# Kernel optimization log

Hardware: AMD Instinct MI355X
Metric: run time of the kernel (lower is better)

The kernel has to match this reference:

```python
import math
import jax, jax.numpy as jnp
import numpy as np

CT = {"SDD": 1000.0, "SCD": 500.0, "det_interval": 1.0, "num_det": 736}


def ramp_filter_np(ct, scale):
    # Standard equiangular fan-beam ramp filter (utility.ramp_filter):
    #   h[0] = 1/(8*db^2); h[n odd] = -1/(2*(pi*sin(n*db))^2); h[n even!=0] = 0
    db = ct["det_interval"] / ct["SDD"] * scale  # angular detector pitch at this scale
    n_det = int(ct["num_det"] // scale)
    n = np.arange(-(n_det - 1), n_det)  # length K = 2*n_det - 1
    h = np.zeros(n.shape, dtype=np.float32)
    h[n == 0] = 1.0 / (8.0 * db ** 2)
    odd = (n % 2) != 0
    h[odd] = -0.5 / (np.pi * np.sin(n[odd] * db)) ** 2
    return h


def setup_inputs() -> dict:
    key = jax.random.key(0)
    scale = 1
    batch, ch, view, det = 16, 1, 1152, CT["num_det"] // scale
    sinogram = jax.random.normal(key, (batch, ch, view, det), dtype=jnp.float32)
    delta_b = CT["det_interval"] / CT["SDD"]
    # recon_filter = ramp_filter * scale * delta_b, shaped [1,1,1,K] (OIHW)
    filt = ramp_filter_np(CT, scale) * scale * delta_b
    recon_filter = jnp.asarray(filt, dtype=jnp.float32)[None, None, None, :]
    return {"sinogram": sinogram, "recon_filter": recon_filter, "scale": scale}


def reference(sinogram, recon_filter, scale):
    det = sinogram.shape[-1]
    # cosine fan-beam pre-weighting
    s_range = (CT["det_interval"]
               * jnp.linspace((1.0 - det) / 2.0, (det - 1.0) / 2.0, det, dtype=jnp.float32)
               * scale) / CT["SDD"]
    cos_weight = (CT["SCD"] / 10000.0) * jnp.cos(s_range)  # [det]
    x = sinogram * cos_weight[None, None, None, :]
    # 1D ramp-filter convolution along detector axis (F.conv2d with 1xK kernel)
    K = recon_filter.shape[-1]
    pad = K // 2
    out = jax.lax.conv_general_dilated(
        x, recon_filter,
        window_strides=(1, 1),
        padding=[(0, 0), (pad, pad)],
        dimension_numbers=("NCHW", "OIHW", "NCHW"),
    )
    return out
```

## Files before the change

### kernel.cpp

```cpp
#include <hip/hip_runtime.h>

typedef unsigned short ushort_t;
typedef ushort_t u16x8 __attribute__((ext_vector_type(8)));
typedef __bf16 bf16x8 __attribute__((ext_vector_type(8)));
typedef float f32x4 __attribute__((ext_vector_type(4)));

#define DET 736
#define NPAD 768
#define NT 23

__device__ __forceinline__ ushort_t f2bf(float f) {
    unsigned u = __builtin_bit_cast(unsigned, f);
    u += 0x7FFFu + ((u >> 16) & 1u);
    return (ushort_t)(u >> 16);
}

__device__ __forceinline__ void gload16(const void* g, void* l) {
    __builtin_amdgcn_global_load_lds(
        (const __attribute__((address_space(1))) unsigned int*)g,
        (__attribute__((address_space(3))) unsigned int*)l,
        16, 0, 0);
}

__global__ void prep_bt(const float* __restrict__ filt, ushort_t* __restrict__ Bt) {
    int idx = blockIdx.x * blockDim.x + threadIdx.x;
    if (idx >= NPAD * DET) return;
    int n = idx / DET;
    int k = idx - n * DET;
    float w = 0.05f * cosf(((float)k - 367.5f) * 0.001f);
    float v = (n < DET) ? filt[k - n + (DET - 1)] * w : 0.0f;
    Bt[idx] = f2bf(v);
}

__global__ __launch_bounds__(256, 4) void gemm_fused(
    const float* __restrict__ A,
    const ushort_t* __restrict__ Bt,
    float* __restrict__ C, int M)
{
    __shared__ ushort_t As[128 * 32];
    __shared__ ushort_t Bs[128 * 32];

    const int tid  = threadIdx.x;
    const int lane = tid & 63;
    const int warp = tid >> 6;
    const int wm   = warp & 1;
    const int wn   = warp >> 1;
    const int quad = lane >> 4;
    const int l16  = lane & 15;

    const size_t row_a0 = (size_t)blockIdx.x * 128;
    const int    row_b0 = blockIdx.y * 128;

    f32x4 acc[4][4];
#pragma unroll
    for (int i = 0; i < 4; ++i)
#pragma unroll
        for (int jx = 0; jx < 4; ++jx)
            acc[i][jx] = (f32x4){0.f, 0.f, 0.f, 0.f};

    const int c0 = tid, c1 = tid + 256;
    const int r0 = c0 >> 2, q0 = c0 & 3;
    const int r1 = c1 >> 2, q1 = c1 & 3;

    const float*    gA0 = A + (row_a0 + r0) * DET + q0 * 8;
    const float*    gA1 = A + (row_a0 + r1) * DET + q1 * 8;
    const ushort_t* gB0 = Bt + (size_t)(row_b0 + r0) * DET + q0 * 8;
    const ushort_t* gB1 = Bt + (size_t)(row_b0 + r1) * DET + q1 * 8;

    f32x4 a0lo = *(const f32x4*)(gA0);
    f32x4 a0hi = *(const f32x4*)(gA0 + 4);
    f32x4 a1lo = *(const f32x4*)(gA1);
    f32x4 a1hi = *(const f32x4*)(gA1 + 4);

    for (int t = 0; t < NT; ++t) {
        __syncthreads();

        u16x8 oa0, oa1;
#pragma unroll
        for (int e = 0; e < 4; ++e) {
            oa0[e]     = f2bf(a0lo[e]);
            oa0[e + 4] = f2bf(a0hi[e]);
            oa1[e]     = f2bf(a1lo[e]);
            oa1[e + 4] = f2bf(a1hi[e]);
        }
        *(u16x8*)(As + c0 * 8) = oa0;
        *(u16x8*)(As + c1 * 8) = oa1;

        const int k0 = t * 32;
        gload16(gB0 + k0, Bs + c0 * 8);
        gload16(gB1 + k0, Bs + c1 * 8);

        __syncthreads();

        if (t + 1 < NT) {
            const int kn = (t + 1) * 32;
            a0lo = *(const f32x4*)(gA0 + kn);
            a0hi = *(const f32x4*)(gA0 + kn + 4);
            a1lo = *(const f32x4*)(gA1 + kn);
            a1hi = *(const f32x4*)(gA1 + kn + 4);
        }

        u16x8 af[4], bfr[4];
#pragma unroll
        for (int mi = 0; mi < 4; ++mi)
            af[mi] = *(const u16x8*)(As + (wm * 64 + mi * 16 + l16) * 32 + quad * 8);
#pragma unroll
        for (int ni = 0; ni < 4; ++ni)
            bfr[ni] = *(const u16x8*)(Bs + (wn * 64 + ni * 16 + l16) * 32 + quad * 8);
#pragma unroll
        for (int mi = 0; mi < 4; ++mi)
#pragma unroll
            for (int ni = 0; ni < 4; ++ni)
                acc[mi][ni] = __builtin_amdgcn_mfma_f32_16x16x32_bf16(
                    __builtin_bit_cast(bf16x8, af[mi]),
                    __builtin_bit_cast(bf16x8, bfr[ni]),
                    acc[mi][ni], 0, 0, 0);
    }

#pragma unroll
    for (int mi = 0; mi < 4; ++mi) {
#pragma unroll
        for (int ni = 0; ni < 4; ++ni) {
            int colg = row_b0 + wn * 64 + ni * 16 + l16;
            if (colg < DET) {
#pragma unroll
                for (int r = 0; r < 4; ++r) {
                    size_t rowg = row_a0 + wm * 64 + mi * 16 + quad * 4 + r;
                    C[rowg * DET + colg] = acc[mi][ni][r];
                }
            }
        }
    }
}

extern "C" void kernel_launch(void* const* d_in, const int* in_sizes, int n_in,
                              void* d_out, int out_size, void* d_ws, size_t ws_size,
                              hipStream_t stream) {
    const float* sino = (const float*)d_in[0];
    const float* filt = (const float*)d_in[1];
    int total = in_sizes[0];
    int M = total / DET;

    ushort_t* Btb = (ushort_t*)d_ws;
    float* out = (float*)d_out;

    prep_bt<<<(NPAD * DET + 255) / 256, 256, 0, stream>>>(filt, Btb);

    dim3 grid(M / 128, NPAD / 128);
    gemm_fused<<<grid, 256, 0, stream>>>(sino, Btb, out, M);
}
```

Before: 132.2 us.

## Double-buffer fp32 A tile in LDS with swizzle, load B fragments directly to registers

The GEMM now stages the fp32 sinogram tile straight into a double-buffered, XOR-swizzled LDS buffer with async global-to-LDS loads. It converts to bf16 at fragment read time and no longer converts in registers before the LDS store. The B (filter matrix) fragments are loaded from global memory directly into registers with a one-step prefetch, skipping LDS. Each K step now needs one barrier instead of two, so loads overlap compute. In exchange, LDS use doubles, register pressure rises, occupancy is lowered to 3 blocks, and each B fragment is read redundantly by the waves that share it.

```diff
diff --git a/kernel.cpp b/kernel.cpp
--- a/kernel.cpp
+++ b/kernel.cpp
@@ -32,13 +32,12 @@
     Bt[idx] = f2bf(v);
 }
 
-__global__ __launch_bounds__(256, 4) void gemm_fused(
+__global__ __launch_bounds__(256, 3) void gemm_fused(
     const float* __restrict__ A,
     const ushort_t* __restrict__ Bt,
     float* __restrict__ C, int M)
 {
-    __shared__ ushort_t As[128 * 32];
-    __shared__ ushort_t Bs[128 * 32];
+    __shared__ float As[2][128 * 32];
 
     const int tid  = threadIdx.x;
     const int lane = tid & 63;
@@ -58,63 +57,76 @@
         for (int jx = 0; jx < 4; ++jx)
             acc[i][jx] = (f32x4){0.f, 0.f, 0.f, 0.f};
 
-    const int c0 = tid, c1 = tid + 256;
-    const int r0 = c0 >> 2, q0 = c0 & 3;
-    const int r1 = c1 >> 2, q1 = c1 & 3;
+    const float* gsrc[4];
+    int          cdst[4];
+#pragma unroll
+    for (int i = 0; i < 4; ++i) {
+        int c    = tid + i * 256;
+        int row  = c >> 3;
+        int part = c & 7;
+        int sp   = part ^ (row & 7);
+        gsrc[i]  = A + (row_a0 + row) * DET + sp * 4;
+        cdst[i]  = c * 4;
+    }
 
-    const float*    gA0 = A + (row_a0 + r0) * DET + q0 * 8;
-    const float*    gA1 = A + (row_a0 + r1) * DET + q1 * 8;
-    const ushort_t* gB0 = Bt + (size_t)(row_b0 + r0) * DET + q0 * 8;
-    const ushort_t* gB1 = Bt + (size_t)(row_b0 + r1) * DET + q1 * 8;
+    const ushort_t* gBp[4];
+#pragma unroll
+    for (int ni = 0; ni < 4; ++ni)
+        gBp[ni] = Bt + (size_t)(row_b0 + wn * 64 + ni * 16 + l16) * DET + quad * 8;
 
-    f32x4 a0lo = *(const f32x4*)(gA0);
-    f32x4 a0hi = *(const f32x4*)(gA0 + 4);
-    f32x4 a1lo = *(const f32x4*)(gA1);
-    f32x4 a1hi = *(const f32x4*)(gA1 + 4);
+    const int r7   = l16 & 7;
+    const int o_lo = ((quad * 2)     ^ r7) * 4;
+    const int o_hi = ((quad * 2 + 1) ^ r7) * 4;
+
+#pragma unroll
+    for (int i = 0; i < 4; ++i)
+        gload16(gsrc[i], &As[0][cdst[i]]);
+    u16x8 bcur[4];
+#pragma unroll
+    for (int ni = 0; ni < 4; ++ni)
+        bcur[ni] = *(const u16x8*)(gBp[ni]);
+    __syncthreads();
 
     for (int t = 0; t < NT; ++t) {
-        __syncthreads();
+        const int cur = t & 1;
+        const int kn  = (t + 1 < NT) ? (t + 1) * 32 : 0;
 
-        u16x8 oa0, oa1;
 #pragma unroll
-        for (int e = 0; e < 4; ++e) {
-            oa0[e]     = f2bf(a0lo[e]);
-            oa0[e + 4] = f2bf(a0hi[e]);
-            oa1[e]     = f2bf(a1lo[e]);
-            oa1[e + 4] = f2bf(a1hi[e]);
-        }
-        *(u16x8*)(As + c0 * 8) = oa0;
-        *(u16x8*)(As + c1 * 8) = oa1;
+        for (int i = 0; i < 4; ++i)
+            gload16(gsrc[i] + kn, &As[cur ^ 1][cdst[i]]);
+        u16x8 bnext[4];
+#pragma unroll
+        for (int ni = 0; ni < 4; ++ni)
+            bnext[ni] = *(const u16x8*)(gBp[ni] + kn);
 
-        const int k0 = t * 32;
-        gload16(gB0 + k0, Bs + c0 * 8);
-        gload16(gB1 + k0, Bs + c1 * 8);
-
-        __syncthreads();
-
-        if (t + 1 < NT) {
-            const int kn = (t + 1) * 32;
-            a0lo = *(const f32x4*)(gA0 + kn);
-            a0hi = *(const f32x4*)(gA0 + kn + 4);
-            a1lo = *(const f32x4*)(gA1 + kn);
-            a1hi = *(const f32x4*)(gA1 + kn + 4);
+        bf16x8 af[4];
+#pragma unroll
+        for (int mi = 0; mi < 4; ++mi) {
+            const int row = wm * 64 + mi * 16 + l16;
+            f32x4 lo = *(const f32x4*)(&As[cur][row * 32 + o_lo]);
+            f32x4 hi = *(const f32x4*)(&As[cur][row * 32 + o_hi]);
+            bf16x8 v;
+#pragma unroll
+            for (int e = 0; e < 4; ++e) {
+                v[e]     = (__bf16)lo[e];
+                v[e + 4] = (__bf16)hi[e];
+            }
+            af[mi] = v;
         }
 
-        u16x8 af[4], bfr[4];
-#pragma unroll
-        for (int mi = 0; mi < 4; ++mi)
-            af[mi] = *(const u16x8*)(As + (wm * 64 + mi * 16 + l16) * 32 + quad * 8);
-#pragma unroll
-        for (int ni = 0; ni < 4; ++ni)
-            bfr[ni] = *(const u16x8*)(Bs + (wn * 64 + ni * 16 + l16) * 32 + quad * 8);
 #pragma unroll
         for (int mi = 0; mi < 4; ++mi)
 #pragma unroll
             for (int ni = 0; ni < 4; ++ni)
                 acc[mi][ni] = __builtin_amdgcn_mfma_f32_16x16x32_bf16(
-                    __builtin_bit_cast(bf16x8, af[mi]),
-                    __builtin_bit_cast(bf16x8, bfr[ni]),
+                    af[mi],
+                    __builtin_bit_cast(bf16x8, bcur[ni]),
                     acc[mi][ni], 0, 0, 0);
+
+        __syncthreads();
+#pragma unroll
+        for (int ni = 0; ni < 4; ++ni)
+            bcur[ni] = bnext[ni];
     }
 
 #pragma unroll
```

Result: slower. 146.8 us (+11.0%).
